# Kernel tuning notes

Hardware: AMD Instinct MI355X
Metric: run time of the kernel (lower is better)

## Reference

```python
import jax, jax.numpy as jnp
import numpy as np

B, C, H, W = 4, 64, 256, 256
P, PRIOR, HID, HEADS, NPROMPT = 4, 64, 128, 4, 4
TOKEN = C * P * P  # 1024
RATIO = 0.25


def _patchify(x):
    b, c, h, w = x.shape
    gh, gw = h // P, w // P
    t = x.reshape(b, c, gh, P, gw, P).transpose(0, 2, 4, 1, 3, 5).reshape(b, gh * gw, c * P * P)
    return t, (b, c, gh, gw)


def _unpatchify(t, meta):
    b, c, gh, gw = meta
    return t.reshape(b, gh, gw, c, P, P).transpose(0, 3, 1, 4, 2, 5).reshape(b, c, gh * P, gw * P)


def _coords(gh, gw):
    ys = (jnp.arange(gh, dtype=jnp.float32) + 0.5) / gh
    xs = (jnp.arange(gw, dtype=jnp.float32) + 0.5) / gw
    yy, xx = jnp.meshgrid(ys, xs, indexing='ij')
    return jnp.stack([yy.ravel(), xx.ravel()], axis=-1)  # [N, 2]


def setup_inputs():
    key = jax.random.key(0)
    ks = iter(jax.random.split(key, 32))
    rn = lambda *s: jax.random.normal(next(ks), s, jnp.float32)
    w = lambda *s: rn(*s) * 0.02
    z = lambda *s: jnp.zeros(s, jnp.float32)
    return dict(
        vis_feat=rn(B, C, H, W),
        ir_feat=rn(B, C, H, W),
        prompt_bank=w(NPROMPT, PRIOR),
        Wr=w(2 * C, NPROMPT), br=z(NPROMPT),
        br_Wtok=w(2, 2 * TOKEN, HID), br_Wpri=w(2, PRIOR, HID), br_Wco=w(2, 2, HID),
        br_bs=z(2, HID), br_Wout=w(2, HID), br_bout=z(2),
        br_Wq=w(2, TOKEN, HID), br_Wk=w(2, TOKEN, HID), br_Wv=w(2, TOKEN, HID),
        br_Wo=w(2, HID, TOKEN), br_Wint=w(2, PRIOR, HID),
        br_Wbyp=w(2, 2 * TOKEN, TOKEN), br_bbyp=z(2, TOKEN),
        conv1_w=w(C, C, 3, 3), conv1_b=z(C),
        conv2_w=w(C, C, 3, 3), conv2_b=z(C),
        Wa1=w(PRIOR, 2 * C), ba1=z(2 * C),
        Wa2=w(2 * C, 2 * C), ba2=z(2 * C),
    )


def reference(vis_feat, ir_feat, prompt_bank, Wr, br, br_Wtok, br_Wpri, br_Wco, br_bs, br_Wout, br_bout, br_Wq, br_Wk, br_Wv, br_Wo, br_Wint, br_Wbyp, br_bbyp, conv1_w, conv1_b, conv2_w, conv2_b, Wa1, ba1, Wa2, ba2):
    # intent router: pooled features -> prompt mixture -> intent vector
    pooled = jnp.concatenate([vis_feat.mean((2, 3)), ir_feat.mean((2, 3))], -1)  # [B, 2C]
    prompt_weight = jax.nn.softmax(pooled @ Wr + br, -1)  # [B, NPROMPT]
    intent = prompt_weight @ prompt_bank  # [B, PRIOR]

    def split(x):
        F = jnp.fft.fft2(x)
        return jnp.abs(F), jnp.angle(F)

    vamp, vph = split(vis_feat)
    iamp, iph = split(ir_feat)

    def fuse(vm, im, i):
        vt, meta = _patchify(vm)
        it_, _ = _patchify(im)
        b, c, gh, gw = meta
        n = gh * gw
        coords = _coords(gh, gw)
        # token score net: tokens + intent + coord embedding -> scalar score per token
        h = (jnp.concatenate([vt, it_], -1) @ br_Wtok[i]
             + (intent @ br_Wpri[i])[:, None, :]
             + (coords @ br_Wco[i])[None] + br_bs[i])
        score = jax.nn.gelu(h) @ br_Wout[i] + br_bout[i]  # [B, N]
        k = max(1, int(n * RATIO))
        topk_val, topk_idx = jax.lax.top_k(score, k)
        gth = lambda t: jnp.take_along_axis(t, topk_idx[:, :, None], axis=1)
        vs, irs = gth(vt), gth(it_)  # [B, k, TOKEN]
        # selected-token cross attention (vis queries, ir keys/values), intent-modulated
        dh = HID // HEADS
        hd = lambda x, Wm: (x @ Wm).reshape(b, k, HEADS, dh)
        q, kk, vv = hd(vs, br_Wq[i]), hd(irs, br_Wk[i]), hd(irs, br_Wv[i])
        attn = jax.nn.softmax(jnp.einsum('bqhd,bkhd->bhqk', q, kk) / jnp.float32(np.sqrt(dh)), -1)
        o = jnp.einsum('bhqk,bkhd->bqhd', attn, vv).reshape(b, k, HID)
        o = o + (intent @ br_Wint[i])[:, None, :]
        fused_sel = vs + o @ br_Wo[i]  # [B, k, TOKEN]
        # lightweight bypass on all tokens (gated blend), then scatter selected back
        g = jax.nn.sigmoid(jnp.concatenate([vt, it_], -1) @ br_Wbyp[i] + br_bbyp[i])
        full = g * vt + (1.0 - g) * it_
        full = full.at[jnp.arange(b)[:, None], topk_idx].set(fused_sel)
        return _unpatchify(full, meta)

    famp = fuse(vamp, iamp, 0)
    fph = fuse(vph, iph, 1)
    fph = jnp.arctan2(jnp.sin(fph), jnp.cos(fph))  # phase wrap to (-pi, pi]
    spec = jax.lax.complex(famp * jnp.cos(fph), famp * jnp.sin(fph))
    spatial = jnp.fft.ifft2(spec).real

    conv = lambda x, wgt, bia: jax.lax.conv_general_dilated(
        x, wgt, (1, 1), 'SAME', dimension_numbers=('NCHW', 'OIHW', 'NCHW')) + bia[None, :, None, None]
    y = conv(jax.nn.relu(conv(spatial, conv1_w, conv1_b)), conv2_w, conv2_b)
    aff = jax.nn.gelu(intent @ Wa1 + ba1) @ Wa2 + ba2  # [B, 2C]
    gamma, beta = aff[:, :C], aff[:, C:]
    y = y * (1.0 + 0.1 * jnp.tanh(gamma))[:, :, None, None] + 0.1 * beta[:, :, None, None]
    return y + 0.5 * (vis_feat + ir_feat)
```

## Files before the change

### kernel.cpp

```cpp
#include <hip/hip_runtime.h>

typedef unsigned int uint;
typedef unsigned long long u64;
typedef __attribute__((ext_vector_type(8))) short short8;
typedef __attribute__((ext_vector_type(4))) float f32x4;

__device__ __forceinline__ uint brev8(uint x){ return __brev(x) >> 24; }
__device__ __forceinline__ float geluf(float x){
  return 0.5f*x*(1.f + tanhf(0.7978845608028654f*(x + 0.044715f*x*x*x)));
}
__device__ __forceinline__ unsigned short f2bf(float f){
  unsigned u = __float_as_uint(f);
  unsigned r = u + 0x7FFFu + ((u >> 16) & 1u);
  return (unsigned short)(r >> 16);
}
__device__ __forceinline__ float bf2f(unsigned short u){
  return __uint_as_float((uint)u << 16);
}

__global__ __launch_bounds__(256) void kern_pool(const float* __restrict__ vis,
                                                 const float* __restrict__ irf,
                                                 float* __restrict__ pooled){
  __shared__ float red[256];
  int bc = blockIdx.x;
  int b = bc >> 7, cc = bc & 127;
  const float* src = (cc < 64) ? (vis + (size_t)(b*64+cc)*65536)
                               : (irf + (size_t)(b*64+(cc-64))*65536);
  float s = 0.f;
  for (int i = threadIdx.x; i < 65536; i += 256) s += src[i];
  red[threadIdx.x] = s;
  __syncthreads();
  for (int off = 128; off > 0; off >>= 1){
    if (threadIdx.x < off) red[threadIdx.x] += red[threadIdx.x + off];
    __syncthreads();
  }
  if (threadIdx.x == 0) pooled[bc] = red[0] * (1.f/65536.f);
}

__global__ __launch_bounds__(256) void kern_small(const float* __restrict__ pooled,
    const float* __restrict__ Wr, const float* __restrict__ br,
    const float* __restrict__ bank, const float* __restrict__ Wpri,
    const float* __restrict__ Wint, const float* __restrict__ Wa1,
    const float* __restrict__ ba1, const float* __restrict__ Wa2,
    const float* __restrict__ ba2,
    float* __restrict__ IP, float* __restrict__ IPint,
    float* __restrict__ modg, float* __restrict__ modb){
  __shared__ float logit_s[16];
  __shared__ float pw_s[16];
  __shared__ float intent_s[4][64];
  __shared__ float t1_s[4][128];
  int t = threadIdx.x;
  if (t < 16){
    int b = t >> 2, j = t & 3;
    float s = br[j];
    for (int k = 0; k < 128; ++k) s += pooled[b*128+k]*Wr[k*4+j];
    logit_s[t] = s;
  }
  __syncthreads();
  if (t < 4){
    int b = t;
    float m = logit_s[b*4];
    for (int j = 1; j < 4; ++j) m = fmaxf(m, logit_s[b*4+j]);
    float e[4], sum = 0.f;
    for (int j = 0; j < 4; ++j){ e[j] = expf(logit_s[b*4+j]-m); sum += e[j]; }
    for (int j = 0; j < 4; ++j) pw_s[b*4+j] = e[j]/sum;
  }
  __syncthreads();
  {
    int b = t >> 6, p = t & 63;
    float s = 0.f;
    for (int j = 0; j < 4; ++j) s += pw_s[b*4+j]*bank[j*64+p];
    intent_s[b][p] = s;
  }
  __syncthreads();
  for (int o = t; o < 1024; o += 256){
    int i = o >> 9, rem = o & 511, b = rem >> 7, n = rem & 127;
    float s1 = 0.f, s2 = 0.f;
    for (int p = 0; p < 64; ++p){
      float iv = intent_s[b][p];
      s1 += iv * Wpri[(i*64+p)*128 + n];
      s2 += iv * Wint[(i*64+p)*128 + n];
    }
    IP[o] = s1; IPint[o] = s2;
  }
  for (int o = t; o < 512; o += 256){
    int b = o >> 7, n = o & 127;
    float s = ba1[n];
    for (int p = 0; p < 64; ++p) s += intent_s[b][p]*Wa1[p*128+n];
    t1_s[b][n] = geluf(s);
  }
  __syncthreads();
  for (int o = t; o < 512; o += 256){
    int b = o >> 7, n = o & 127;
    float s = ba2[n];
    for (int p = 0; p < 128; ++p) s += t1_s[b][p]*Wa2[p*128+n];
    if (n < 64) modg[b*64+n] = 1.f + 0.1f*tanhf(s);
    else        modb[b*64+(n-64)] = 0.1f*s;
  }
}

__global__ __launch_bounds__(256) void kern_fft_rows_fwd(const float* __restrict__ x,
    float* __restrict__ sre, float* __restrict__ sim){
  __shared__ float re[2][256], im[2][256];
  __shared__ float twr[128], twi[128];
  int t = threadIdx.x;
  if (t < 128){
    float a = -6.2831853071795864f * (float)t * (1.f/256.f);
    sincosf(a, &twi[t], &twr[t]);
  }
  int r = t >> 7, jj = t & 127;
  size_t row = (size_t)blockIdx.x*2 + r;
  {
    const float* xp = x + row*256;
    re[r][jj] = xp[jj]; re[r][jj+128] = xp[jj+128];
    im[r][jj] = 0.f;    im[r][jj+128] = 0.f;
  }
  __syncthreads();
  for (int s = 0; s < 8; ++s){
    int half = 128 >> s;
    int j = jj & (half-1);
    int g = jj >> (7-s);
    int k = (g << (8-s)) + j;
    int m = j << s;
    float wc = twr[m], ws = twi[m];
    float are = re[r][k],      aim = im[r][k];
    float bre = re[r][k+half], bim = im[r][k+half];
    re[r][k] = are + bre; im[r][k] = aim + bim;
    float tr = are - bre, ti = aim - bim;
    re[r][k+half] = tr*wc - ti*ws;
    im[r][k+half] = tr*ws + ti*wc;
    __syncthreads();
  }
  {
    float* orp = sre + row*256; float* oip = sim + row*256;
    int w1 = jj, w2 = jj + 128;
    orp[w1] = re[r][brev8(w1)]; oip[w1] = im[r][brev8(w1)];
    orp[w2] = re[r][brev8(w2)]; oip[w2] = im[r][brev8(w2)];
  }
}

__global__ __launch_bounds__(256) void kern_ifft_rows_spec(const float* __restrict__ famp,
    const float* __restrict__ fph, float* __restrict__ sre, float* __restrict__ sim){
  __shared__ float re[4][256], im[4][256];
  __shared__ float twr[128], twi[128];
  int t = threadIdx.x;
  if (t < 128){
    float a = -6.2831853071795864f * (float)t * (1.f/256.f);
    sincosf(a, &twi[t], &twr[t]);
  }
  int R = blockIdx.x * 4;
  {
    int r = t >> 6, q = t & 63;
    int row = R + r;
    int bc = row >> 8, h = row & 255;
    int b = bc >> 6, c = bc & 63;
    size_t addr = ((size_t)(b*4096 + (h>>2)*64 + q))*1024 + c*16 + (h&3)*4;
    float4 a4 = *(const float4*)(famp + addr);
    float4 p4 = *(const float4*)(fph + addr);
    float sn, cs;
    sincosf(p4.x, &sn, &cs); re[r][4*q+0] = a4.x*cs; im[r][4*q+0] = a4.x*sn;
    sincosf(p4.y, &sn, &cs); re[r][4*q+1] = a4.y*cs; im[r][4*q+1] = a4.y*sn;
    sincosf(p4.z, &sn, &cs); re[r][4*q+2] = a4.z*cs; im[r][4*q+2] = a4.z*sn;
    sincosf(p4.w, &sn, &cs); re[r][4*q+3] = a4.w*cs; im[r][4*q+3] = a4.w*sn;
  }
  __syncthreads();
  for (int s = 0; s < 8; ++s){
    int half = 128 >> s;
    #pragma unroll
    for (int bi0 = 0; bi0 < 2; ++bi0){
      int bi = t + bi0*256;
      int r = bi >> 7, tj = bi & 127;
      int j = tj & (half-1);
      int g = tj >> (7-s);
      int k = (g << (8-s)) + j;
      int m = j << s;
      float wc = twr[m], ws = -twi[m];
      float are = re[r][k],      aim = im[r][k];
      float bre = re[r][k+half], bim = im[r][k+half];
      re[r][k] = are + bre; im[r][k] = aim + bim;
      float tr = are - bre, ti = aim - bim;
      re[r][k+half] = tr*wc - ti*ws;
      im[r][k+half] = tr*ws + ti*wc;
    }
    __syncthreads();
  }
  {
    int r = t >> 6, q = t & 63;
    size_t row = (size_t)R + r;
    float4 vr, vi;
    vr.x = re[r][brev8(4*q+0)]; vi.x = im[r][brev8(4*q+0)];
    vr.y = re[r][brev8(4*q+1)]; vi.y = im[r][brev8(4*q+1)];
    vr.z = re[r][brev8(4*q+2)]; vi.z = im[r][brev8(4*q+2)];
    vr.w = re[r][brev8(4*q+3)]; vi.w = im[r][brev8(4*q+3)];
    *(float4*)(sre + row*256 + 4*q) = vr;
    *(float4*)(sim + row*256 + 4*q) = vi;
  }
}

template<int DIR>
__global__ __launch_bounds__(256) void kern_fft_cols(const float* __restrict__ sre,
    const float* __restrict__ sim, void* __restrict__ out0, void* __restrict__ out1){
  __shared__ float reL[256*17];
  __shared__ float imL[256*17];
  __shared__ float twr[128], twi[128];
  int t = threadIdx.x;
  if (t < 128){
    float a = -6.2831853071795864f * (float)t * (1.f/256.f);
    sincosf(a, &twi[t], &twr[t]);
  }
  int img = blockIdx.x >> 4;
  int c0 = (blockIdx.x & 15) * 16;
  {
    const float* pr = sre + ((size_t)img*256 + t)*256 + c0;
    const float* pi = sim + ((size_t)img*256 + t)*256 + c0;
    #pragma unroll
    for (int p = 0; p < 4; ++p){
      float4 vr = *(const float4*)(pr + 4*p);
      float4 vi = *(const float4*)(pi + 4*p);
      int base = t*17 + 4*p;
      reL[base+0]=vr.x; reL[base+1]=vr.y; reL[base+2]=vr.z; reL[base+3]=vr.w;
      imL[base+0]=vi.x; imL[base+1]=vi.y; imL[base+2]=vi.z; imL[base+3]=vi.w;
    }
  }
  __syncthreads();
  int col = t & 15, tb = t >> 4;
  for (int s = 0; s < 8; ++s){
    int half = 128 >> s;
    #pragma unroll
    for (int it = 0; it < 8; ++it){
      int tj = tb + it*16;
      int j = tj & (half-1);
      int g = tj >> (7-s);
      int k = (g << (8-s)) + j;
      int m = j << s;
      float wc = twr[m];
      float ws = (DIR == 0) ? twi[m] : -twi[m];
      int i0 = k*17 + col, i1 = (k+half)*17 + col;
      float are = reL[i0], aim = imL[i0];
      float bre = reL[i1], bim = imL[i1];
      reL[i0] = are + bre; imL[i0] = aim + bim;
      float tr = are - bre, ti = aim - bim;
      reL[i1] = tr*wc - ti*ws;
      imL[i1] = tr*ws + ti*wc;
    }
    __syncthreads();
  }
  int b = img >> 6, c = img & 63;
  int h = t; int src = (int)brev8((uint)h);
  if (DIR == 0){
    unsigned short* oa = (unsigned short*)out0;
    unsigned short* op = (unsigned short*)out1;
    int gy = h >> 2, py = h & 3;
    #pragma unroll
    for (int p = 0; p < 4; ++p){
      int base = src*17 + 4*p;
      float a0, a1, a2, a3, p0, p1, p2, p3;
      float rr, ii;
      rr = reL[base+0]; ii = imL[base+0]; a0 = sqrtf(rr*rr+ii*ii); p0 = atan2f(ii, rr);
      rr = reL[base+1]; ii = imL[base+1]; a1 = sqrtf(rr*rr+ii*ii); p1 = atan2f(ii, rr);
      rr = reL[base+2]; ii = imL[base+2]; a2 = sqrtf(rr*rr+ii*ii); p2 = atan2f(ii, rr);
      rr = reL[base+3]; ii = imL[base+3]; a3 = sqrtf(rr*rr+ii*ii); p3 = atan2f(ii, rr);
      size_t addr = ((size_t)(b*4096 + gy*64 + (c0>>2) + p))*1024 + c*16 + py*4;
      uint2 av, pv;
      av.x = (uint)f2bf(a0) | ((uint)f2bf(a1) << 16);
      av.y = (uint)f2bf(a2) | ((uint)f2bf(a3) << 16);
      pv.x = (uint)f2bf(p0) | ((uint)f2bf(p1) << 16);
      pv.y = (uint)f2bf(p2) | ((uint)f2bf(p3) << 16);
      *(uint2*)(oa + addr) = av;
      *(uint2*)(op + addr) = pv;
    }
  } else {
    float* op = (float*)out0 + ((size_t)img*256 + h)*256 + c0;
    #pragma unroll
    for (int p = 0; p < 4; ++p){
      int base = src*17 + 4*p;
      float4 v;
      v.x = reL[base+0]*(1.f/65536.f);
      v.y = reL[base+1]*(1.f/65536.f);
      v.z = reL[base+2]*(1.f/65536.f);
      v.w = reL[base+3]*(1.f/65536.f);
      *(float4*)(op + 4*p) = v;
    }
  }
}

struct TRS {
  const float* src[10];
  unsigned short* dst[10];
  int K[10], N[10];
  int start[11];
};
__global__ __launch_bounds__(256) void kern_tr(TRS p){
  __shared__ float lds[32][33];
  int bid = blockIdx.x;
  int e = 0;
  while (bid >= p.start[e+1]) ++e;
  int tloc = bid - p.start[e];
  int tilesN = p.N[e] >> 5;
  int tn = tloc % tilesN, tk = tloc / tilesN;
  int k0 = tk << 5, n0 = tn << 5;
  const float* src = p.src[e];
  unsigned short* dst = p.dst[e];
  int K = p.K[e], N = p.N[e];
  int r = threadIdx.x >> 5, c = threadIdx.x & 31;
  #pragma unroll
  for (int i = 0; i < 4; ++i)
    lds[r + 8*i][c] = src[(size_t)(k0 + r + 8*i)*N + n0 + c];
  __syncthreads();
  #pragma unroll
  for (int i = 0; i < 4; ++i)
    dst[(size_t)(n0 + r + 8*i)*K + k0 + c] = f2bf(lds[c][r + 8*i]);
}

struct GP2 {
  const unsigned short* A0[6];
  const unsigned short* A1[2];
  const unsigned short* Bt[6];
  float* Cm[6];
  const int* idxp[6];
  const float* ep0[2];
  const float* ep1[2];
  const float* ep2[2];
  int N, K;
};

template<int AMODE, int EPI>
__global__ __launch_bounds__(256) void kern_mgemm2(GP2 p){
  __shared__ __align__(16) unsigned short Asb[64*64];
  __shared__ __align__(16) unsigned short Bsb[128*64];
  __shared__ int idx_s[64];
  int z = blockIdx.z;
  const unsigned short* A0 = p.A0[z];
  const unsigned short* Bt = p.Bt[z];
  float* Cm = p.Cm[z];
  int tid = threadIdx.x;
  int m0 = blockIdx.x * 64;
  int n0 = blockIdx.y * 128;
  int lane = tid & 63, w = tid >> 6;
  int wr = w & 1, wc = w >> 1;
  int lr = lane & 15, ql = lane >> 4;

  if (AMODE == 2){
    if (tid < 64){
      int m = m0 + tid;
      idx_s[tid] = p.idxp[z][(m >> 10)*1024 + (m & 1023)];
    }
    __syncthreads();
  }
  int gb = m0 >> 10;

  f32x4 acc[2][4];
  #pragma unroll
  for (int i = 0; i < 2; ++i)
    #pragma unroll
    for (int j = 0; j < 4; ++j) acc[i][j] = (f32x4){0.f,0.f,0.f,0.f};

  int kh = tid & 7;
  int rA = tid >> 3;
  for (int k0 = 0; k0 < p.K; k0 += 64){
    #pragma unroll
    for (int s = 0; s < 2; ++s){
      int m = rA + 32*s;
      const unsigned short* ap;
      if (AMODE == 1){
        const unsigned short* srcp = (k0 < 1024) ? A0 : p.A1[z];
        ap = srcp + (size_t)(m0+m)*1024 + (k0 & 1023) + kh*8;
      } else {
        ap = A0 + ((size_t)(gb << 12) + idx_s[m])*(size_t)p.K + k0 + kh*8;
      }
      short8 v = *(const short8*)ap;
      int byte = m*128 + ((kh*16) ^ ((m & 7)*16));
      *(short8*)((char*)Asb + byte) = v;
    }
    #pragma unroll
    for (int s = 0; s < 4; ++s){
      int n = rA + 32*s;
      short8 v = *(const short8*)(Bt + (size_t)(n0+n)*p.K + k0 + kh*8);
      int byte = n*128 + ((kh*16) ^ ((n & 7)*16));
      *(short8*)((char*)Bsb + byte) = v;
    }
    __syncthreads();
    short8 af[2][2], bf[4][2];
    #pragma unroll
    for (int fm = 0; fm < 2; ++fm){
      int row = wr*32 + fm*16 + lr;
      #pragma unroll
      for (int kq = 0; kq < 2; ++kq){
        int byte = row*128 + ((kq*64 + ql*16) ^ ((row & 7)*16));
        af[fm][kq] = *(const short8*)((const char*)Asb + byte);
      }
    }
    #pragma unroll
    for (int fn = 0; fn < 4; ++fn){
      int row = wc*64 + fn*16 + lr;
      #pragma unroll
      for (int kq = 0; kq < 2; ++kq){
        int byte = row*128 + ((kq*64 + ql*16) ^ ((row & 7)*16));
        bf[fn][kq] = *(const short8*)((const char*)Bsb + byte);
      }
    }
    #pragma unroll
    for (int kq = 0; kq < 2; ++kq)
      #pragma unroll
      for (int fm = 0; fm < 2; ++fm)
        #pragma unroll
        for (int fn = 0; fn < 4; ++fn)
          acc[fm][fn] = __builtin_amdgcn_mfma_f32_16x16x32_bf16(af[fm][kq], bf[fn][kq],
                                                                acc[fm][fn], 0, 0, 0);
    __syncthreads();
  }

  #pragma unroll
  for (int fm = 0; fm < 2; ++fm){
    #pragma unroll
    for (int fn = 0; fn < 4; ++fn){
      int n = n0 + wc*64 + fn*16 + lr;
      #pragma unroll
      for (int reg = 0; reg < 4; ++reg){
        int m = m0 + wr*32 + fm*16 + ql*4 + reg;
        float v = acc[fm][fn][reg];
        if (EPI == 0){
          Cm[(size_t)m*p.N + n] = v;
        } else {
          int bl = m >> 12, g = m & 4095;
          int gy = g >> 6, gx = g & 63;
          float cy = ((float)gy + 0.5f)*(1.f/64.f);
          float cx = ((float)gx + 0.5f)*(1.f/64.f);
          float o = v + p.ep0[z][bl*128 + n] + cy*p.ep1[z][n]
                  + cx*p.ep1[z][128 + n] + p.ep2[z][n];
          Cm[(size_t)m*128 + n] = o;
        }
      }
    }
  }
}

struct GP3 {
  const unsigned short* A0[2];
  const unsigned short* A1[2];
  const unsigned short* Bt[2];
  float* Cm[2];
  const float* bias[2];
  const unsigned short* vt[2];
  const unsigned short* it[2];
  int K;
};

__global__ __launch_bounds__(256) void kern_mgemm3(GP3 p){
  __shared__ __align__(16) unsigned short Asb[128*64];
  __shared__ __align__(16) unsigned short Bsb[128*64];
  int z = blockIdx.z;
  const unsigned short* Bt = p.Bt[z];
  float* Cm = p.Cm[z];
  int tid = threadIdx.x;
  int m0 = blockIdx.x * 128;
  int n0 = blockIdx.y * 128;
  int lane = tid & 63, w = tid >> 6;
  int wr = w & 1, wc = w >> 1;
  int lr = lane & 15, ql = lane >> 4;

  f32x4 acc[4][4];
  #pragma unroll
  for (int i = 0; i < 4; ++i)
    #pragma unroll
    for (int j = 0; j < 4; ++j) acc[i][j] = (f32x4){0.f,0.f,0.f,0.f};

  int kh = tid & 7;
  int rA = tid >> 3;
  for (int k0 = 0; k0 < p.K; k0 += 64){
    const unsigned short* Asrc = (k0 < 1024) ? p.A0[z] : p.A1[z];
    int kk = (k0 & 1023) + kh*8;
    #pragma unroll
    for (int s = 0; s < 4; ++s){
      int m = rA + 32*s;
      short8 v = *(const short8*)(Asrc + (size_t)(m0+m)*1024 + kk);
      int byte = m*128 + ((kh*16) ^ ((m & 7)*16));
      *(short8*)((char*)Asb + byte) = v;
    }
    #pragma unroll
    for (int s = 0; s < 4; ++s){
      int n = rA + 32*s;
      short8 v = *(const short8*)(Bt + (size_t)(n0+n)*p.K + k0 + kh*8);
      int byte = n*128 + ((kh*16) ^ ((n & 7)*16));
      *(short8*)((char*)Bsb + byte) = v;
    }
    __syncthreads();
    short8 af[4][2], bf[4][2];
    #pragma unroll
    for (int fm = 0; fm < 4; ++fm){
      int row = wr*64 + fm*16 + lr;
      #pragma unroll
      for (int kq = 0; kq < 2; ++kq){
        int byte = row*128 + ((kq*64 + ql*16) ^ ((row & 7)*16));
        af[fm][kq] = *(const short8*)((const char*)Asb + byte);
      }
    }
    #pragma unroll
    for (int fn = 0; fn < 4; ++fn){
      int row = wc*64 + fn*16 + lr;
      #pragma unroll
      for (int kq = 0; kq < 2; ++kq){
        int byte = row*128 + ((kq*64 + ql*16) ^ ((row & 7)*16));
        bf[fn][kq] = *(const short8*)((const char*)Bsb + byte);
      }
    }
    #pragma unroll
    for (int kq = 0; kq < 2; ++kq)
      #pragma unroll
      for (int fm = 0; fm < 4; ++fm)
        #pragma unroll
        for (int fn = 0; fn < 4; ++fn)
          acc[fm][fn] = __builtin_amdgcn_mfma_f32_16x16x32_bf16(af[fm][kq], bf[fn][kq],
                                                                acc[fm][fn], 0, 0, 0);
    __syncthreads();
  }

  const unsigned short* vtp = p.vt[z];
  const unsigned short* itp = p.it[z];
  #pragma unroll
  for (int fm = 0; fm < 4; ++fm){
    #pragma unroll
    for (int fn = 0; fn < 4; ++fn){
      int n = n0 + wc*64 + fn*16 + lr;
      float bia = p.bias[z][n];
      #pragma unroll
      for (int reg = 0; reg < 4; ++reg){
        int m = m0 + wr*64 + fm*16 + ql*4 + reg;
        size_t off = (size_t)m*1024 + n;
        float vt = bf2f(vtp[off]);
        float it = bf2f(itp[off]);
        float gg = 1.f/(1.f + expf(-(acc[fm][fn][reg] + bia)));
        Cm[off] = gg*vt + (1.f-gg)*it;
      }
    }
  }
}

struct SCP {
  const float* A0[2];
  const float* Bm[2];
  float* Cm[2];
  const int* idxp[2];
  const unsigned short* vtb[2];
};

__global__ __launch_bounds__(256) void kern_scat(SCP p){
  __shared__ __align__(16) unsigned short Asb[64*40];
  __shared__ __align__(16) unsigned short Bsb[128*40];
  __shared__ int idx_s[64];
  int z = blockIdx.z;
  const float* A0 = p.A0[z];
  const float* Bm = p.Bm[z];
  float* Cm = p.Cm[z];
  int tid = threadIdx.x;
  int m0 = blockIdx.y * 64;
  int n0 = blockIdx.x * 128;
  int lane = tid & 63, w = tid >> 6;
  int wr = w & 1, wc = w >> 1;
  int lr = lane & 15, ql = lane >> 4;
  if (tid < 64){
    int m = m0 + tid;
    idx_s[tid] = p.idxp[z][(m >> 10)*1024 + (m & 1023)];
  }
  __syncthreads();
  int gb = m0 >> 10;

  f32x4 acc[2][4];
  #pragma unroll
  for (int i = 0; i < 2; ++i)
    #pragma unroll
    for (int j = 0; j < 4; ++j) acc[i][j] = (f32x4){0.f,0.f,0.f,0.f};

  for (int k0 = 0; k0 < 128; k0 += 32){
    {
      int m = tid & 63;
      int khh = (tid >> 6) * 8;
      const float* ap = A0 + (size_t)(m0+m)*128 + k0 + khh;
      float4 f0 = *(const float4*)ap;
      float4 f1 = *(const float4*)(ap + 4);
      short8 v;
      v[0]=(short)f2bf(f0.x); v[1]=(short)f2bf(f0.y);
      v[2]=(short)f2bf(f0.z); v[3]=(short)f2bf(f0.w);
      v[4]=(short)f2bf(f1.x); v[5]=(short)f2bf(f1.y);
      v[6]=(short)f2bf(f1.z); v[7]=(short)f2bf(f1.w);
      *(short8*)&Asb[m*40 + khh] = v;
    }
    #pragma unroll
    for (int e0 = 0; e0 < 512; e0 += 256){
      int e = e0 + tid;
      int n = e & 127;
      int khh = (e >> 7) * 8;
      const float* bp = Bm + (size_t)(k0+khh)*1024 + n0 + n;
      short8 v;
      #pragma unroll
      for (int j = 0; j < 8; ++j) v[j] = (short)f2bf(bp[(size_t)j*1024]);
      *(short8*)&Bsb[n*40 + khh] = v;
    }
    __syncthreads();
    short8 af[2], bf[4];
    #pragma unroll
    for (int fr = 0; fr < 2; ++fr)
      af[fr] = *(const short8*)&Asb[(wr*32 + fr*16 + lr)*40 + ql*8];
    #pragma unroll
    for (int fc = 0; fc < 4; ++fc)
      bf[fc] = *(const short8*)&Bsb[(wc*64 + fc*16 + lr)*40 + ql*8];
    #pragma unroll
    for (int fr = 0; fr < 2; ++fr)
      #pragma unroll
      for (int fc = 0; fc < 4; ++fc)
        acc[fr][fc] = __builtin_amdgcn_mfma_f32_16x16x32_bf16(af[fr], bf[fc],
                                                              acc[fr][fc], 0, 0, 0);
    __syncthreads();
  }

  #pragma unroll
  for (int fr = 0; fr < 2; ++fr){
    #pragma unroll
    for (int fc = 0; fc < 4; ++fc){
      int n = n0 + wc*64 + fc*16 + lr;
      #pragma unroll
      for (int reg = 0; reg < 4; ++reg){
        int mloc = wr*32 + fr*16 + ql*4 + reg;
        int gt = idx_s[mloc];
        size_t off = ((size_t)(gb << 12) + gt)*1024 + n;
        Cm[off] = acc[fr][fc][reg] + bf2f(p.vtb[z][off]);
      }
    }
  }
}

__global__ __launch_bounds__(64) void kern_score(const float* __restrict__ h,
// ... 57 lines not shown
  float oa[32];
  #pragma unroll
  for (int d = 0; d < 32; ++d) oa[d] = 0.f;
  for (int kt = 0; kt < 4; ++kt){
    int k0 = c*256 + kt*64;
    #pragma unroll
    for (int rep = 0; rep < 4; ++rep){
      int f = t + rep*128;
      int r = f >> 3, q4 = f & 7;
      size_t base = boff + (size_t)(k0 + r)*128 + hh*32 + 4*q4;
      *(float4*)&Ks[r][4*q4] = *(const float4*)(kb + base);
      *(float4*)&Vs[r][4*q4] = *(const float4*)(vb + base);
    }
    __syncthreads();
    #pragma unroll
    for (int st = 0; st < 4; ++st){
      float s[16];
      #pragma unroll
      for (int j = 0; j < 16; ++j){
        float v = 0.f;
        #pragma unroll
        for (int d = 0; d < 32; ++d) v += qv[d]*Ks[st*16+j][d];
        s[j] = v * 0.17677669529663687f;
      }
      float mt = s[0];
      #pragma unroll
      for (int j = 1; j < 16; ++j) mt = fmaxf(mt, s[j]);
      float mnew = fmaxf(mrun, mt);
      float alpha = expf(mrun - mnew);
      lrun *= alpha;
      #pragma unroll
      for (int d = 0; d < 32; ++d) oa[d] *= alpha;
      #pragma unroll
      for (int j = 0; j < 16; ++j){
        float pe = expf(s[j] - mnew);
        lrun += pe;
        #pragma unroll
        for (int d = 0; d < 32; ++d) oa[d] += pe*Vs[st*16+j][d];
      }
      mrun = mnew;
    }
    __syncthreads();
  }
  size_t rec = (((size_t)zf*4 + hh)*4 + c)*1024 + jq;
  float* pp = paoa + rec*32;
  #pragma unroll
  for (int d = 0; d < 8; ++d) ((float4*)pp)[d] = ((float4*)oa)[d];
  pml[rec*2]   = mrun;
  pml[rec*2+1] = lrun;
}

__global__ __launch_bounds__(256) void kern_attn_comb(const float* __restrict__ paoa,
    const float* __restrict__ pml, float* __restrict__ ob,
    const float* __restrict__ ipint, int PB, int b0){
  int t = threadIdx.x;
  int hh = blockIdx.y, zf = blockIdx.z;
  int jq = blockIdx.x*256 + t;
  size_t rbase = (((size_t)zf*4 + hh)*4)*1024 + jq;
  float mc[4], lc[4];
  #pragma unroll
  for (int c = 0; c < 4; ++c){
    mc[c] = pml[(rbase + c*1024)*2];
    lc[c] = pml[(rbase + c*1024)*2 + 1];
  }
  float M = fmaxf(fmaxf(mc[0], mc[1]), fmaxf(mc[2], mc[3]));
  float wgt[4], L = 0.f;
  #pragma unroll
  for (int c = 0; c < 4; ++c){ wgt[c] = expf(mc[c] - M); L += lc[c]*wgt[c]; }
  float inv = 1.f/L;
  int br = (zf >= PB) ? 1 : 0;
  int bb = zf - br*PB;
  const float* ip = ipint + br*512 + (b0+bb)*128 + hh*32;
  float* op = ob + (size_t)zf*131072 + (size_t)jq*128 + hh*32;
  #pragma unroll
  for (int d = 0; d < 32; ++d){
    float o = 0.f;
    #pragma unroll
    for (int c = 0; c < 4; ++c) o += paoa[(rbase + c*1024)*32 + d]*wgt[c];
    op[d] = o*inv + ip[d];
  }
}

__global__ __launch_bounds__(256) void kern_wt(const float* __restrict__ w1,
    const float* __restrict__ w2, unsigned short* __restrict__ wt){
  int blk = blockIdx.x;
  const float* src = (blk < 9) ? w1 : w2;
  int tap = blk - (blk < 9 ? 0 : 9);
  unsigned short* dst = wt + (blk < 9 ? 0 : 36864) + tap*4096;
  for (int e = threadIdx.x; e < 4096; e += 256){
    dst[e] = f2bf(src[(size_t)e*9 + tap]);
  }
}

template<int MODE>
__global__ __launch_bounds__(256) void kern_cmfma(const float* __restrict__ in,
    const unsigned short* __restrict__ wt, const float* __restrict__ bias,
    float* __restrict__ out,
    const float* __restrict__ modg, const float* __restrict__ modb,
    const float* __restrict__ vis, const float* __restrict__ irf){
  __shared__ __align__(16) unsigned short ins[64][268];
  int t = threadIdx.x;
  int y = blockIdx.x, b = blockIdx.y;
  int lane = t & 63, w = t >> 6;
  int wc = w & 1, wx = w >> 1;
  int lr = lane & 15, ql = lane >> 4;

  f32x4 acc[2][8];
  #pragma unroll
  for (int f = 0; f < 2; ++f)
    #pragma unroll
    for (int xf = 0; xf < 8; ++xf) acc[f][xf] = (f32x4){0.f,0.f,0.f,0.f};

  for (int dy = 0; dy < 3; ++dy){
    int yy = y + dy - 1;
    if (yy < 0 || yy > 255) continue;
    const float* src = in + ((size_t)(b*64)*256 + yy)*256;
    #pragma unroll
    for (int s = 0; s < 16; ++s){
      int e = t + s*256;
      int ci = e >> 6, q = e & 63;
      float4 f4 = *(const float4*)(src + (size_t)ci*65536 + 4*q);
      uint lo = (uint)f2bf(f4.x) | ((uint)f2bf(f4.y) << 16);
      uint hi = (uint)f2bf(f4.z) | ((uint)f2bf(f4.w) << 16);
      *(uint2*)&ins[ci][4*q + 4] = make_uint2(lo, hi);
    }
    if (t < 128){
      int r = t & 63;
      ins[r][(t >> 6) ? 260 : 3] = 0;
    }
    __syncthreads();
    short8 wf[2][3][2];
    #pragma unroll
    for (int kk = 0; kk < 2; ++kk)
      #pragma unroll
      for (int dx = 0; dx < 3; ++dx)
        #pragma unroll
        for (int f = 0; f < 2; ++f)
          wf[kk][dx][f] = *(const short8*)(wt +
            (size_t)((dy*3 + dx)*64 + 32*wc + 16*f + lr)*64 + kk*32 + ql*8);
    #pragma unroll
    for (int kk = 0; kk < 2; ++kk){
      const unsigned short* bp = &ins[kk*32 + ql*8][0];
      #pragma unroll
      for (int dx = 0; dx < 3; ++dx){
        int xb = 128*wx + lr + dx + 3;
        #pragma unroll
        for (int xf = 0; xf < 8; ++xf){
          int xi = xb + 16*xf;
          short8 bf;
          #pragma unroll
          for (int e = 0; e < 8; ++e) bf[e] = (short)bp[e*268 + xi];
          acc[0][xf] = __builtin_amdgcn_mfma_f32_16x16x32_bf16(wf[kk][dx][0], bf,
                                                               acc[0][xf], 0, 0, 0);
          acc[1][xf] = __builtin_amdgcn_mfma_f32_16x16x32_bf16(wf[kk][dx][1], bf,
                                                               acc[1][xf], 0, 0, 0);
        }
      }
    }
    __syncthreads();
  }

  #pragma unroll
  for (int f = 0; f < 2; ++f){
    #pragma unroll
    for (int xf = 0; xf < 8; ++xf){
      int x = 128*wx + 16*xf + lr;
      #pragma unroll
      for (int reg = 0; reg < 4; ++reg){
        int co = 32*wc + 16*f + ql*4 + reg;
        float v = acc[f][xf][reg] + bias[co];
        size_t oi = ((size_t)(b*64 + co)*256 + y)*256 + x;
        if (MODE == 1){
          out[oi] = fmaxf(v, 0.f);
        } else {
          out[oi] = v*modg[b*64+co] + modb[b*64+co] + 0.5f*(vis[oi] + irf[oi]);
        }
      }
    }
  }
}

extern "C" void kernel_launch(void* const* d_in, const int* in_sizes, int n_in,
                              void* d_out, int out_size, void* d_ws, size_t ws_size,
                              hipStream_t stream){
  (void)in_sizes; (void)n_in; (void)out_size;
  const float* vis  = (const float*)d_in[0];
  const float* irf  = (const float*)d_in[1];
  const float* bank = (const float*)d_in[2];
  const float* Wr   = (const float*)d_in[3];
  const float* br   = (const float*)d_in[4];
  const float* Wtok = (const float*)d_in[5];
  const float* Wpri = (const float*)d_in[6];
  const float* Wco  = (const float*)d_in[7];
  const float* bs   = (const float*)d_in[8];
  const float* Wout = (const float*)d_in[9];
  const float* bout = (const float*)d_in[10];
  const float* Wq   = (const float*)d_in[11];
  const float* Wk   = (const float*)d_in[12];
  const float* Wv   = (const float*)d_in[13];
  const float* Wo   = (const float*)d_in[14];
  const float* Wint = (const float*)d_in[15];
  const float* Wbyp = (const float*)d_in[16];
  const float* bbyp = (const float*)d_in[17];
  const float* c1w  = (const float*)d_in[18];
  const float* c1b  = (const float*)d_in[19];
  const float* c2w  = (const float*)d_in[20];
  const float* c2b  = (const float*)d_in[21];
  const float* Wa1  = (const float*)d_in[22];
  const float* ba1  = (const float*)d_in[23];
  const float* Wa2  = (const float*)d_in[24];
  const float* ba2  = (const float*)d_in[25];

  auto needB = [](int PB)->size_t{
    return ((size_t)PB*14755840 + 2792448) * 4;
  };
  const int PB = (ws_size >= needB(4)) ? 4 : (ws_size >= needB(2)) ? 2 : 1;

  float* ws = (float*)d_ws;
  const size_t PLF = (size_t)PB*4194304;
  float* PH4 = ws;
  unsigned short* ABV = (unsigned short*)(ws + PLF);
  unsigned short* PBV = ABV + PLF;
  unsigned short* ABI = PBV + PLF;
  unsigned short* PBI = ABI + PLF;
  float* S0 = ws + PLF;
  float* S1 = S0 + PLF;
  float* sm = ws + 3*PLF;
  float* hbuf  = sm; sm += (size_t)2*PB*524288;
  float* qbuf  = sm; sm += (size_t)2*PB*131072;
  float* kbuf  = sm; sm += (size_t)2*PB*131072;
  float* vbuf  = sm; sm += (size_t)2*PB*131072;
  float* obuf  = sm; sm += (size_t)2*PB*131072;
  float* score = sm; sm += (size_t)2*PB*4096;
  int*   idxb  = (int*)sm; sm += (size_t)2*PB*1024;
  float* pml   = sm; sm += (size_t)PB*65536;
  unsigned short* BTtok = (unsigned short*)sm;
  unsigned short* BTbyp = BTtok + 524288;
  unsigned short* BTq   = BTbyp + 4194304;
  unsigned short* BTk   = BTq + 262144;
  unsigned short* BTv   = BTk + 262144;
  sm += 2752512;
  float* pooled= sm; sm += 512;
  float* IP    = sm; sm += 1024;
  float* IPint = sm; sm += 1024;
  float* modg  = sm; sm += 256;
  float* modb  = sm; sm += 256;
  unsigned short* wtb = (unsigned short*)sm; sm += 36864;
  float* paoa = hbuf;

  kern_pool <<<512, 256, 0, stream>>>(vis, irf, pooled);
  kern_small<<<1, 256, 0, stream>>>(pooled, Wr, br, bank, Wpri, Wint,
                                    Wa1, ba1, Wa2, ba2, IP, IPint, modg, modb);
  kern_wt   <<<18, 256, 0, stream>>>(c1w, c2w, wtb);
  {
    TRS tr{};
    const float* srcs[10] = {Wtok, Wtok+262144, Wbyp, Wbyp+2097152,
                             Wq, Wq+131072, Wk, Wk+131072, Wv, Wv+131072};
    unsigned short* dsts[10] = {BTtok, BTtok+262144, BTbyp, BTbyp+2097152,
                                BTq, BTq+131072, BTk, BTk+131072, BTv, BTv+131072};
    int Ks[10] = {2048,2048,2048,2048,1024,1024,1024,1024,1024,1024};
    int Ns[10] = {128,128,1024,1024,128,128,128,128,128,128};
    int tiles[10] = {256,256,2048,2048,128,128,128,128,128,128};
    int acc0 = 0;
    for (int i = 0; i < 10; ++i){
      tr.src[i] = srcs[i]; tr.dst[i] = dsts[i];
      tr.K[i] = Ks[i]; tr.N[i] = Ns[i];
      tr.start[i] = acc0; acc0 += tiles[i];
    }
    tr.start[10] = acc0;
    kern_tr<<<acc0, 256, 0, stream>>>(tr);
  }

  for (int b0 = 0; b0 < 4; b0 += PB){
    const float* vis_b = vis + (size_t)b0*4194304;
    const float* ir_b  = irf + (size_t)b0*4194304;
    float* OUT = (float*)d_out + (size_t)b0*4194304;

    kern_fft_rows_fwd<<<PB*8192, 256, 0, stream>>>(vis_b, OUT, PH4);
    kern_fft_cols<0> <<<PB*1024, 256, 0, stream>>>(OUT, PH4, ABV, PBV);
    kern_fft_rows_fwd<<<PB*8192, 256, 0, stream>>>(ir_b, OUT, PH4);
    kern_fft_cols<0> <<<PB*1024, 256, 0, stream>>>(OUT, PH4, ABI, PBI);

    {
      GP2 p{};
      p.A0[0]=ABV; p.A1[0]=ABI; p.A0[1]=PBV; p.A1[1]=PBI;
      for (int z = 0; z < 2; ++z){
        p.Bt[z] = BTtok + (size_t)z*262144;
        p.Cm[z] = hbuf + (size_t)z*PB*524288;
        p.ep0[z] = IP + z*512 + b0*128;
        p.ep1[z] = Wco + z*256;
        p.ep2[z] = bs + z*128;
      }
      p.N = 128; p.K = 2048;
      kern_mgemm2<1,1><<<dim3(PB*64, 1, 2), 256, 0, stream>>>(p);
    }
    kern_score<<<dim3(PB*4096, 2), 64, 0, stream>>>(hbuf, Wout, bout, score, PB*4096);
    kern_topk <<<2*PB, 1024, 0, stream>>>(score, idxb);
    {
      GP3 p{};
      p.A0[0]=ABV; p.A1[0]=ABI; p.A0[1]=PBV; p.A1[1]=PBI;
      p.vt[0]=ABV; p.it[0]=ABI; p.vt[1]=PBV; p.it[1]=PBI;
      p.Cm[0]=OUT; p.Cm[1]=PH4;
      for (int z = 0; z < 2; ++z){
        p.Bt[z] = BTbyp + (size_t)z*2097152;
        p.bias[z] = bbyp + z*1024;
      }
      p.K = 2048;
      kern_mgemm3<<<dim3(PB*32, 8, 2), 256, 0, stream>>>(p);
    }
    {
      GP2 p{};
      const unsigned short* Aplanes[6] = {ABV, ABI, ABI, PBV, PBI, PBI};
      const unsigned short* Bmats[6] = {BTq, BTk, BTv,
                                        BTq+131072, BTk+131072, BTv+131072};
      float* Cms[6] = {qbuf, kbuf, vbuf,
                       qbuf+(size_t)PB*131072, kbuf+(size_t)PB*131072,
                       vbuf+(size_t)PB*131072};
      for (int z = 0; z < 6; ++z){
        p.A0[z] = Aplanes[z]; p.Bt[z] = Bmats[z]; p.Cm[z] = Cms[z];
        p.idxp[z] = idxb + (z < 3 ? 0 : PB*1024);
      }
      p.N = 128; p.K = 1024;
      kern_mgemm2<2,0><<<dim3(PB*16, 1, 6), 256, 0, stream>>>(p);
    }
    kern_attn_part<<<dim3(8, 4, 2*PB*4), 128, 0, stream>>>(qbuf, kbuf, vbuf,
                                                           paoa, pml);
    kern_attn_comb<<<dim3(4, 4, 2*PB), 256, 0, stream>>>(paoa, pml, obuf,
                                                         IPint, PB, b0);
    {
      SCP p{};
      p.A0[0]=obuf; p.A0[1]=obuf+(size_t)PB*131072;
      p.Bm[0]=Wo; p.Bm[1]=Wo+131072;
      p.Cm[0]=OUT; p.Cm[1]=PH4;
      p.vtb[0]=ABV; p.vtb[1]=PBV;
      p.idxp[0]=idxb; p.idxp[1]=idxb+PB*1024;
      kern_scat<<<dim3(8, PB*16, 2), 256, 0, stream>>>(p);
    }

    kern_ifft_rows_spec<<<PB*4096, 256, 0, stream>>>(OUT, PH4, S0, S1);
    kern_fft_cols<1>   <<<PB*1024, 256, 0, stream>>>(S0, S1, OUT, nullptr);
  }

  kern_cmfma<1><<<dim3(256, 4), 256, 0, stream>>>((float*)d_out, wtb, c1b, ws,
                                                  nullptr, nullptr, nullptr, nullptr);
  kern_cmfma<2><<<dim3(256, 4), 256, 0, stream>>>(ws, wtb + 36864, c2b, (float*)d_out,
                                                  modg, modb, vis, irf);
}
```

Measured before the change: 1.419 ms.

## Store FFT row intermediates in bf16 and fold bypass GEMM into mgemm2

The row FFT outputs (forward and inverse) now go to global memory as packed bf16 instead of fp32, which halves the intermediate traffic between the row and column FFT passes. The column FFT loads them with short8 vectors and converts back to float in shared memory. Separately, the dedicated 128x128 bypass GEMM kernel is removed and replaced by a new epilogue mode of the 64-row mgemm2 kernel, which computes the sigmoid-gated blend. The bf16 intermediates cost precision in the spectrum, and the smaller GEMM tile changes how much data each tile reuses.

```diff
diff --git a/kernel.cpp b/kernel.cpp
--- a/kernel.cpp
+++ b/kernel.cpp
@@ -1,6 +1,7 @@
 #include <hip/hip_runtime.h>
 
 typedef unsigned int uint;
+typedef unsigned short ushort;
 typedef unsigned long long u64;
 typedef __attribute__((ext_vector_type(8))) short short8;
 typedef __attribute__((ext_vector_type(4))) float f32x4;
@@ -9,12 +10,12 @@
 __device__ __forceinline__ float geluf(float x){
   return 0.5f*x*(1.f + tanhf(0.7978845608028654f*(x + 0.044715f*x*x*x)));
 }
-__device__ __forceinline__ unsigned short f2bf(float f){
+__device__ __forceinline__ ushort f2bf(float f){
   unsigned u = __float_as_uint(f);
   unsigned r = u + 0x7FFFu + ((u >> 16) & 1u);
-  return (unsigned short)(r >> 16);
-}
-__device__ __forceinline__ float bf2f(unsigned short u){
+  return (ushort)(r >> 16);
+}
+__device__ __forceinline__ float bf2f(ushort u){
   return __uint_as_float((uint)u << 16);
 }
 
@@ -100,7 +101,7 @@
 }
 
 __global__ __launch_bounds__(256) void kern_fft_rows_fwd(const float* __restrict__ x,
-    float* __restrict__ sre, float* __restrict__ sim){
+    ushort* __restrict__ sre, ushort* __restrict__ sim){
   __shared__ float re[2][256], im[2][256];
   __shared__ float twr[128], twi[128];
   int t = threadIdx.x;
@@ -132,15 +133,16 @@
     __syncthreads();
   }
   {
-    float* orp = sre + row*256; float* oip = sim + row*256;
-    int w1 = jj, w2 = jj + 128;
-    orp[w1] = re[r][brev8(w1)]; oip[w1] = im[r][brev8(w1)];
-    orp[w2] = re[r][brev8(w2)]; oip[w2] = im[r][brev8(w2)];
+    int e0 = 2*jj;
+    uint vr = (uint)f2bf(re[r][brev8(e0)]) | ((uint)f2bf(re[r][brev8(e0+1)]) << 16);
+    uint vi = (uint)f2bf(im[r][brev8(e0)]) | ((uint)f2bf(im[r][brev8(e0+1)]) << 16);
+    *(uint*)(sre + row*256 + e0) = vr;
+    *(uint*)(sim + row*256 + e0) = vi;
   }
 }
 
 __global__ __launch_bounds__(256) void kern_ifft_rows_spec(const float* __restrict__ famp,
-    const float* __restrict__ fph, float* __restrict__ sre, float* __restrict__ sim){
+    const float* __restrict__ fph, ushort* __restrict__ sre, ushort* __restrict__ sim){
   __shared__ float re[4][256], im[4][256];
   __shared__ float twr[128], twi[128];
   int t = threadIdx.x;
@@ -187,19 +189,19 @@
   {
     int r = t >> 6, q = t & 63;
     size_t row = (size_t)R + r;
-    float4 vr, vi;
-    vr.x = re[r][brev8(4*q+0)]; vi.x = im[r][brev8(4*q+0)];
-    vr.y = re[r][brev8(4*q+1)]; vi.y = im[r][brev8(4*q+1)];
-    vr.z = re[r][brev8(4*q+2)]; vi.z = im[r][brev8(4*q+2)];
-    vr.w = re[r][brev8(4*q+3)]; vi.w = im[r][brev8(4*q+3)];
-    *(float4*)(sre + row*256 + 4*q) = vr;
-    *(float4*)(sim + row*256 + 4*q) = vi;
+    uint2 vr, vi;
+    vr.x = (uint)f2bf(re[r][brev8(4*q+0)]) | ((uint)f2bf(re[r][brev8(4*q+1)]) << 16);
+    vr.y = (uint)f2bf(re[r][brev8(4*q+2)]) | ((uint)f2bf(re[r][brev8(4*q+3)]) << 16);
+    vi.x = (uint)f2bf(im[r][brev8(4*q+0)]) | ((uint)f2bf(im[r][brev8(4*q+1)]) << 16);
+    vi.y = (uint)f2bf(im[r][brev8(4*q+2)]) | ((uint)f2bf(im[r][brev8(4*q+3)]) << 16);
+    *(uint2*)(sre + row*256 + 4*q) = vr;
+    *(uint2*)(sim + row*256 + 4*q) = vi;
   }
 }
 
 template<int DIR>
-__global__ __launch_bounds__(256) void kern_fft_cols(const float* __restrict__ sre,
-    const float* __restrict__ sim, void* __restrict__ out0, void* __restrict__ out1){
+__global__ __launch_bounds__(256) void kern_fft_cols(const ushort* __restrict__ sre,
+    const ushort* __restrict__ sim, void* __restrict__ out0, void* __restrict__ out1){
   __shared__ float reL[256*17];
   __shared__ float imL[256*17];
   __shared__ float twr[128], twi[128];
@@ -211,15 +213,19 @@
   int img = blockIdx.x >> 4;
   int c0 = (blockIdx.x & 15) * 16;
   {
-    const float* pr = sre + ((size_t)img*256 + t)*256 + c0;
-    const float* pi = sim + ((size_t)img*256 + t)*256 + c0;
-    #pragma unroll
-    for (int p = 0; p < 4; ++p){
-      float4 vr = *(const float4*)(pr + 4*p);
-      float4 vi = *(const float4*)(pi + 4*p);
-      int base = t*17 + 4*p;
-      reL[base+0]=vr.x; reL[base+1]=vr.y; reL[base+2]=vr.z; reL[base+3]=vr.w;
-      imL[base+0]=vi.x; imL[base+1]=vi.y; imL[base+2]=vi.z; imL[base+3]=vi.w;
+    const ushort* pr = sre + ((size_t)img*256 + t)*256 + c0;
+    const ushort* pi = sim + ((size_t)img*256 + t)*256 + c0;
+    short8 r0 = *(const short8*)pr;
+    short8 r1 = *(const short8*)(pr + 8);
+    short8 i0 = *(const short8*)pi;
+    short8 i1 = *(const short8*)(pi + 8);
+    int base = t*17;
+    #pragma unroll
+    for (int j = 0; j < 8; ++j){
+      reL[base+j]   = bf2f((ushort)r0[j]);
+      reL[base+8+j] = bf2f((ushort)r1[j]);
+      imL[base+j]   = bf2f((ushort)i0[j]);
+      imL[base+8+j] = bf2f((ushort)i1[j]);
     }
   }
   __syncthreads();
@@ -248,8 +254,8 @@
   int b = img >> 6, c = img & 63;
   int h = t; int src = (int)brev8((uint)h);
   if (DIR == 0){
-    unsigned short* oa = (unsigned short*)out0;
-    unsigned short* op = (unsigned short*)out1;
+    ushort* oa = (ushort*)out0;
+    ushort* op = (ushort*)out1;
     int gy = h >> 2, py = h & 3;
     #pragma unroll
     for (int p = 0; p < 4; ++p){
@@ -286,7 +292,7 @@
 
 struct TRS {
   const float* src[10];
-  unsigned short* dst[10];
+  ushort* dst[10];
   int K[10], N[10];
   int start[11];
 };
@@ -300,7 +306,7 @@
   int tn = tloc % tilesN, tk = tloc / tilesN;
   int k0 = tk << 5, n0 = tn << 5;
   const float* src = p.src[e];
-  unsigned short* dst = p.dst[e];
+  ushort* dst = p.dst[e];
   int K = p.K[e], N = p.N[e];
   int r = threadIdx.x >> 5, c = threadIdx.x & 31;
   #pragma unroll
@@ -313,25 +319,27 @@
 }
 
 struct GP2 {
-  const unsigned short* A0[6];
-  const unsigned short* A1[2];
-  const unsigned short* Bt[6];
+  const ushort* A0[6];
+  const ushort* A1[2];
+  const ushort* Bt[6];
   float* Cm[6];
   const int* idxp[6];
   const float* ep0[2];
   const float* ep1[2];
   const float* ep2[2];
+  const ushort* vt[2];
+  const ushort* it[2];
   int N, K;
 };
 
 template<int AMODE, int EPI>
 __global__ __launch_bounds__(256) void kern_mgemm2(GP2 p){
-  __shared__ __align__(16) unsigned short Asb[64*64];
-  __shared__ __align__(16) unsigned short Bsb[128*64];
+  __shared__ __align__(16) ushort Asb[64*64];
+  __shared__ __align__(16) ushort Bsb[128*64];
   __shared__ int idx_s[64];
   int z = blockIdx.z;
-  const unsigned short* A0 = p.A0[z];
-  const unsigned short* Bt = p.Bt[z];
+  const ushort* A0 = p.A0[z];
+  const ushort* Bt = p.Bt[z];
   float* Cm = p.Cm[z];
   int tid = threadIdx.x;
   int m0 = blockIdx.x * 64;
@@ -361,9 +369,9 @@
     #pragma unroll
     for (int s = 0; s < 2; ++s){
       int m = rA + 32*s;
-      const unsigned short* ap;
+      const ushort* ap;
       if (AMODE == 1){
-        const unsigned short* srcp = (k0 < 1024) ? A0 : p.A1[z];
+        const ushort* srcp = (k0 < 1024) ? A0 : p.A1[z];
         ap = srcp + (size_t)(m0+m)*1024 + (k0 & 1023) + kh*8;
       } else {
         ap = A0 + ((size_t)(gb << 12) + idx_s[m])*(size_t)p.K + k0 + kh*8;
@@ -421,7 +429,7 @@
         float v = acc[fm][fn][reg];
         if (EPI == 0){
           Cm[(size_t)m*p.N + n] = v;
-        } else {
+        } else if (EPI == 1){
           int bl = m >> 12, g = m & 4095;
           int gy = g >> 6, gx = g & 63;
           float cy = ((float)gy + 0.5f)*(1.f/64.f);
@@ -429,108 +437,13 @@
           float o = v + p.ep0[z][bl*128 + n] + cy*p.ep1[z][n]
                   + cx*p.ep1[z][128 + n] + p.ep2[z][n];
           Cm[(size_t)m*128 + n] = o;
+        } else {
+          size_t off = (size_t)m*1024 + n;
+          float vt = bf2f(p.vt[z][off]);
+          float it = bf2f(p.it[z][off]);
+          float gg = 1.f/(1.f + expf(-(v + p.ep0[z][n])));
+          Cm[off] = gg*vt + (1.f-gg)*it;
         }
-      }
-    }
-  }
-}
-
-struct GP3 {
-  const unsigned short* A0[2];
-  const unsigned short* A1[2];
-  const unsigned short* Bt[2];
-  float* Cm[2];
-  const float* bias[2];
-  const unsigned short* vt[2];
-  const unsigned short* it[2];
-  int K;
-};
-
-__global__ __launch_bounds__(256) void kern_mgemm3(GP3 p){
-  __shared__ __align__(16) unsigned short Asb[128*64];
-  __shared__ __align__(16) unsigned short Bsb[128*64];
-  int z = blockIdx.z;
-  const unsigned short* Bt = p.Bt[z];
-  float* Cm = p.Cm[z];
-  int tid = threadIdx.x;
-  int m0 = blockIdx.x * 128;
-  int n0 = blockIdx.y * 128;
-  int lane = tid & 63, w = tid >> 6;
-  int wr = w & 1, wc = w >> 1;
-  int lr = lane & 15, ql = lane >> 4;
-
-  f32x4 acc[4][4];
-  #pragma unroll
-  for (int i = 0; i < 4; ++i)
-    #pragma unroll
-    for (int j = 0; j < 4; ++j) acc[i][j] = (f32x4){0.f,0.f,0.f,0.f};
-
-  int kh = tid & 7;
-  int rA = tid >> 3;
-  for (int k0 = 0; k0 < p.K; k0 += 64){
-    const unsigned short* Asrc = (k0 < 1024) ? p.A0[z] : p.A1[z];
-    int kk = (k0 & 1023) + kh*8;
-    #pragma unroll
-    for (int s = 0; s < 4; ++s){
-      int m = rA + 32*s;
-      short8 v = *(const short8*)(Asrc + (size_t)(m0+m)*1024 + kk);
-      int byte = m*128 + ((kh*16) ^ ((m & 7)*16));
-      *(short8*)((char*)Asb + byte) = v;
-    }
-    #pragma unroll
-    for (int s = 0; s < 4; ++s){
-      int n = rA + 32*s;
-      short8 v = *(const short8*)(Bt + (size_t)(n0+n)*p.K + k0 + kh*8);
-      int byte = n*128 + ((kh*16) ^ ((n & 7)*16));
-      *(short8*)((char*)Bsb + byte) = v;
-    }
-    __syncthreads();
-    short8 af[4][2], bf[4][2];
-    #pragma unroll
-    for (int fm = 0; fm < 4; ++fm){
-      int row = wr*64 + fm*16 + lr;
-      #pragma unroll
-      for (int kq = 0; kq < 2; ++kq){
-        int byte = row*128 + ((kq*64 + ql*16) ^ ((row & 7)*16));
-        af[fm][kq] = *(const short8*)((const char*)Asb + byte);
-      }
-    }
-    #pragma unroll
-    for (int fn = 0; fn < 4; ++fn){
-      int row = wc*64 + fn*16 + lr;
-      #pragma unroll
-      for (int kq = 0; kq < 2; ++kq){
-        int byte = row*128 + ((kq*64 + ql*16) ^ ((row & 7)*16));
-        bf[fn][kq] = *(const short8*)((const char*)Bsb + byte);
-      }
-    }
-    #pragma unroll
-    for (int kq = 0; kq < 2; ++kq)
-      #pragma unroll
-      for (int fm = 0; fm < 4; ++fm)
-        #pragma unroll
-        for (int fn = 0; fn < 4; ++fn)
-          acc[fm][fn] = __builtin_amdgcn_mfma_f32_16x16x32_bf16(af[fm][kq], bf[fn][kq],
-                                                                acc[fm][fn], 0, 0, 0);
-    __syncthreads();
-  }
-
-  const unsigned short* vtp = p.vt[z];
-  const unsigned short* itp = p.it[z];
-  #pragma unroll
-  for (int fm = 0; fm < 4; ++fm){
-    #pragma unroll
-    for (int fn = 0; fn < 4; ++fn){
-      int n = n0 + wc*64 + fn*16 + lr;
-      float bia = p.bias[z][n];
-      #pragma unroll
-      for (int reg = 0; reg < 4; ++reg){
-        int m = m0 + wr*64 + fm*16 + ql*4 + reg;
-        size_t off = (size_t)m*1024 + n;
-        float vt = bf2f(vtp[off]);
-        float it = bf2f(itp[off]);
-        float gg = 1.f/(1.f + expf(-(acc[fm][fn][reg] + bia)));
-        Cm[off] = gg*vt + (1.f-gg)*it;
       }
     }
   }
@@ -541,12 +454,12 @@
   const float* Bm[2];
   float* Cm[2];
   const int* idxp[2];
-  const unsigned short* vtb[2];
+  const ushort* vtb[2];
 };
 
 __global__ __launch_bounds__(256) void kern_scat(SCP p){
-  __shared__ __align__(16) unsigned short Asb[64*40];
-  __shared__ __align__(16) unsigned short Bsb[128*40];
+  __shared__ __align__(16) ushort Asb[64*40];
+  __shared__ __align__(16) ushort Bsb[128*40];
   __shared__ int idx_s[64];
   int z = blockIdx.z;
   const float* A0 = p.A0[z];
@@ -770,11 +683,11 @@
 }
 
 __global__ __launch_bounds__(256) void kern_wt(const float* __restrict__ w1,
-    const float* __restrict__ w2, unsigned short* __restrict__ wt){
+    const float* __restrict__ w2, ushort* __restrict__ wt){
   int blk = blockIdx.x;
   const float* src = (blk < 9) ? w1 : w2;
   int tap = blk - (blk < 9 ? 0 : 9);
-  unsigned short* dst = wt + (blk < 9 ? 0 : 36864) + tap*4096;
+  ushort* dst = wt + (blk < 9 ? 0 : 36864) + tap*4096;
   for (int e = threadIdx.x; e < 4096; e += 256){
     dst[e] = f2bf(src[(size_t)e*9 + tap]);
   }
@@ -782,11 +695,11 @@
 
 template<int MODE>
 __global__ __launch_bounds__(256) void kern_cmfma(const float* __restrict__ in,
-    const unsigned short* __restrict__ wt, const float* __restrict__ bias,
+    const ushort* __restrict__ wt, const float* __restrict__ bias,
     float* __restrict__ out,
     const float* __restrict__ modg, const float* __restrict__ modb,
     const float* __restrict__ vis, const float* __restrict__ irf){
-  __shared__ __align__(16) unsigned short ins[64][268];
+  __shared__ __align__(16) ushort ins[64][268];
   int t = threadIdx.x;
   int y = blockIdx.x, b = blockIdx.y;
   int lane = t & 63, w = t >> 6;
@@ -828,7 +741,7 @@
             (size_t)((dy*3 + dx)*64 + 32*wc + 16*f + lr)*64 + kk*32 + ql*8);
     #pragma unroll
     for (int kk = 0; kk < 2; ++kk){
-      const unsigned short* bp = &ins[kk*32 + ql*8][0];
+      const ushort* bp = &ins[kk*32 + ql*8][0];
       #pragma unroll
       for (int dx = 0; dx < 3; ++dx){
         int xb = 128*wx + lr + dx + 3;
@@ -906,13 +819,15 @@
 
   float* ws = (float*)d_ws;
   const size_t PLF = (size_t)PB*4194304;
-  float* PH4 = ws;
-  unsigned short* ABV = (unsigned short*)(ws + PLF);
-  unsigned short* PBV = ABV + PLF;
-  unsigned short* ABI = PBV + PLF;
-  unsigned short* PBI = ABI + PLF;
-  float* S0 = ws + PLF;
-  float* S1 = S0 + PLF;
+  ushort* FRre = (ushort*)ws;
+  ushort* FRim = FRre + PLF;
+  float*  PH4  = ws;
+  ushort* ABV = (ushort*)(ws + PLF);
+  ushort* PBV = ABV + PLF;
+  ushort* ABI = PBV + PLF;
+  ushort* PBI = ABI + PLF;
+  ushort* IRre = ABV;
+  ushort* IRim = ABV + PLF;
   float* sm = ws + 3*PLF;
   float* hbuf  = sm; sm += (size_t)2*PB*524288;
   float* qbuf  = sm; sm += (size_t)2*PB*131072;
@@ -922,18 +837,18 @@
   float* score = sm; sm += (size_t)2*PB*4096;
   int*   idxb  = (int*)sm; sm += (size_t)2*PB*1024;
   float* pml   = sm; sm += (size_t)PB*65536;
-  unsigned short* BTtok = (unsigned short*)sm;
-  unsigned short* BTbyp = BTtok + 524288;
-  unsigned short* BTq   = BTbyp + 4194304;
-  unsigned short* BTk   = BTq + 262144;
-  unsigned short* BTv   = BTk + 262144;
+  ushort* BTtok = (ushort*)sm;
+  ushort* BTbyp = BTtok + 524288;
+  ushort* BTq   = BTbyp + 4194304;
+  ushort* BTk   = BTq + 262144;
+  ushort* BTv   = BTk + 262144;
   sm += 2752512;
   float* pooled= sm; sm += 512;
   float* IP    = sm; sm += 1024;
   float* IPint = sm; sm += 1024;
   float* modg  = sm; sm += 256;
   float* modb  = sm; sm += 256;
-  unsigned short* wtb = (unsigned short*)sm; sm += 36864;
+  ushort* wtb = (ushort*)sm; sm += 36864;
   float* paoa = hbuf;
 
   kern_pool <<<512, 256, 0, stream>>>(vis, irf, pooled);
@@ -944,8 +859,8 @@
     TRS tr{};
     const float* srcs[10] = {Wtok, Wtok+262144, Wbyp, Wbyp+2097152,
                              Wq, Wq+131072, Wk, Wk+131072, Wv, Wv+131072};
-    unsigned short* dsts[10] = {BTtok, BTtok+262144, BTbyp, BTbyp+2097152,
-                                BTq, BTq+131072, BTk, BTk+131072, BTv, BTv+131072};
+    ushort* dsts[10] = {BTtok, BTtok+262144, BTbyp, BTbyp+2097152,
+                        BTq, BTq+131072, BTk, BTk+131072, BTv, BTv+131072};
     int Ks[10] = {2048,2048,2048,2048,1024,1024,1024,1024,1024,1024};
     int Ns[10] = {128,128,1024,1024,128,128,128,128,128,128};
     int tiles[10] = {256,256,2048,2048,128,128,128,128,128,128};
@@ -964,10 +879,10 @@
     const float* ir_b  = irf + (size_t)b0*4194304;
     float* OUT = (float*)d_out + (size_t)b0*4194304;
 
-    kern_fft_rows_fwd<<<PB*8192, 256, 0, stream>>>(vis_b, OUT, PH4);
-    kern_fft_cols<0> <<<PB*1024, 256, 0, stream>>>(OUT, PH4, ABV, PBV);
-    kern_fft_rows_fwd<<<PB*8192, 256, 0, stream>>>(ir_b, OUT, PH4);
-    kern_fft_cols<0> <<<PB*1024, 256, 0, stream>>>(OUT, PH4, ABI, PBI);
+    kern_fft_rows_fwd<<<PB*8192, 256, 0, stream>>>(vis_b, FRre, FRim);
+    kern_fft_cols<0> <<<PB*1024, 256, 0, stream>>>(FRre, FRim, ABV, PBV);
+    kern_fft_rows_fwd<<<PB*8192, 256, 0, stream>>>(ir_b, FRre, FRim);
+    kern_fft_cols<0> <<<PB*1024, 256, 0, stream>>>(FRre, FRim, ABI, PBI);
 
     {
       GP2 p{};
@@ -985,22 +900,21 @@
     kern_score<<<dim3(PB*4096, 2), 64, 0, stream>>>(hbuf, Wout, bout, score, PB*4096);
     kern_topk <<<2*PB, 1024, 0, stream>>>(score, idxb);
     {
-      GP3 p{};
+      GP2 p{};
       p.A0[0]=ABV; p.A1[0]=ABI; p.A0[1]=PBV; p.A1[1]=PBI;
       p.vt[0]=ABV; p.it[0]=ABI; p.vt[1]=PBV; p.it[1]=PBI;
       p.Cm[0]=OUT; p.Cm[1]=PH4;
       for (int z = 0; z < 2; ++z){
         p.Bt[z] = BTbyp + (size_t)z*2097152;
-        p.bias[z] = bbyp + z*1024;
-      }
-      p.K = 2048;
-      kern_mgemm3<<<dim3(PB*32, 8, 2), 256, 0, stream>>>(p);
+        p.ep0[z] = bbyp + z*1024;
+      }
+      p.N = 1024; p.K = 2048;
+      kern_mgemm2<1,2><<<dim3(PB*64, 8, 2), 256, 0, stream>>>(p);
     }
     {
       GP2 p{};
-      const unsigned short* Aplanes[6] = {ABV, ABI, ABI, PBV, PBI, PBI};
-      const unsigned short* Bmats[6] = {BTq, BTk, BTv,
-                                        BTq+131072, BTk+131072, BTv+131072};
+      const ushort* Aplanes[6] = {ABV, ABI, ABI, PBV, PBI, PBI};
+      const ushort* Bmats[6] = {BTq, BTk, BTv, BTq+131072, BTk+131072, BTv+131072};
       float* Cms[6] = {qbuf, kbuf, vbuf,
                        qbuf+(size_t)PB*131072, kbuf+(size_t)PB*131072,
                        vbuf+(size_t)PB*131072};
@@ -1025,8 +939,8 @@
       kern_scat<<<dim3(8, PB*16, 2), 256, 0, stream>>>(p);
     }
 
-    kern_ifft_rows_spec<<<PB*4096, 256, 0, stream>>>(OUT, PH4, S0, S1);
-    kern_fft_cols<1>   <<<PB*1024, 256, 0, stream>>>(S0, S1, OUT, nullptr);
+    kern_ifft_rows_spec<<<PB*4096, 256, 0, stream>>>(OUT, PH4, IRre, IRim);
+    kern_fft_cols<1>   <<<PB*1024, 256, 0, stream>>>(IRre, IRim, OUT, nullptr);
   }
 
   kern_cmfma<1><<<dim3(256, 4), 256, 0, stream>>>((float*)d_out, wtb, c1b, ws,
```

New measurement: 1.474 ms. 1.04x slower.
